# Performance work log

Hardware: AMD Instinct MI355X
Metric: run time of the kernel (lower is better)

The kernel has to match this reference:

```python
import jax, jax.numpy as jnp
import numpy as np

D_MODEL = 1024
TDS = 64
B, S = 8, 2048
DIN = D_MODEL + TDS   # 1088
DH = D_MODEL // 2     # 512


def setup_inputs() -> dict:
    key = jax.random.key(0)
    ks = jax.random.split(key, 6)
    sc = 1.0 / np.sqrt(DIN)
    return {
        "time_features": jax.random.normal(ks[0], (B, S, D_MODEL), jnp.float32),
        "env_info": jax.random.normal(ks[1], (B, TDS), jnp.float32),
        "Wq": jax.random.normal(ks[2], (DIN, DH), jnp.float32) * sc,
        "bq": jnp.zeros((DH,), jnp.float32),
        "Wk": jax.random.normal(ks[3], (DIN, DH), jnp.float32) * sc,
        "bk": jnp.zeros((DH,), jnp.float32),
        "Wv": jax.random.normal(ks[4], (DIN, DH), jnp.float32) * sc,
        "bv": jnp.zeros((DH,), jnp.float32),
        "Wg": jax.random.normal(ks[5], (DIN, 1), jnp.float32) * sc,
        "bg": jnp.zeros((1,), jnp.float32),
    }


def reference(time_features, env_info, Wq, bq, Wk, bk, Wv, bv, Wg, bg):
    b, s, _ = time_features.shape
    env = jnp.broadcast_to(env_info[:, None, :], (b, s, env_info.shape[-1]))
    x = jnp.concatenate([time_features, env], axis=2)  # [B,S,DIN]
    q = x @ Wq + bq                                    # [B,S,DH]
    k = x @ Wk + bk
    v = x @ Wv + bv
    gate = jax.nn.sigmoid(x @ Wg + bg)                 # [B,S,1]
    scores = jnp.einsum('bqd,bkd->bqk', q, k) / jnp.sqrt(jnp.float32(D_MODEL))
    gated = scores * gate                              # gate broadcasts over key dim
    attn = jax.nn.softmax(gated, axis=-1)
    return jnp.einsum('bqk,bkd->bqd', attn, v)         # [B,S,DH]
```

## Files before the change

kernel.cpp:

```cpp
#include <hip/hip_runtime.h>
#include <stdint.h>

typedef __attribute__((ext_vector_type(8))) __bf16 bf16x8;
typedef __attribute__((ext_vector_type(4))) __bf16 bf16x4;
typedef __attribute__((ext_vector_type(4))) float  f32x4;

#define DEV __device__ __forceinline__

DEV void gload16(const void* g, void* l) {
  __builtin_amdgcn_global_load_lds((const __attribute__((address_space(1))) uint32_t*)g,
                                   (__attribute__((address_space(3))) uint32_t*)l,
                                   16, 0, 0);
}

DEV f32x4 mfma16(bf16x8 a, bf16x8 b, f32x4 c) {
  return __builtin_amdgcn_mfma_f32_16x16x32_bf16(a, b, c, 0, 0, 0);
}

#define XB_OFF   0UL
#define S_OFF    0UL
#define Q_OFF    35651584UL
#define K_OFF    52428800UL
#define V_OFF    69206016UL
#define VT_OFF   85983232UL
#define WT_OFF   102760448UL
#define BIAS_OFF 106102784UL
#define GATE_OFF 106108928UL
#define S8_OFF   106174464UL

__global__ __launch_bounds__(256) void k_xbgate(
    const float* __restrict__ tf, const float* __restrict__ env,
    const float* __restrict__ Wg, const float* __restrict__ bg,
    __bf16* __restrict__ xb, float* __restrict__ gate) {
  const int row = blockIdx.x;
  const int t   = threadIdx.x;
  const int b   = row >> 11;
  const float4 v  = ((const float4*)(tf + (size_t)row * 1024))[t];
  const float4 wv = ((const float4*)Wg)[t];
  float dot = v.x * wv.x + v.y * wv.y + v.z * wv.z + v.w * wv.w;
  bf16x4 o; o.x = (__bf16)v.x; o.y = (__bf16)v.y; o.z = (__bf16)v.z; o.w = (__bf16)v.w;
  *(bf16x4*)(xb + (size_t)row * 1088 + t * 4) = o;
  if (t < 16) {
    const float4 e  = ((const float4*)(env + b * 64))[t];
    const float4 we = ((const float4*)Wg)[256 + t];
    dot += e.x * we.x + e.y * we.y + e.z * we.z + e.w * we.w;
    bf16x4 oe; oe.x = (__bf16)e.x; oe.y = (__bf16)e.y; oe.z = (__bf16)e.z; oe.w = (__bf16)e.w;
    *(bf16x4*)(xb + (size_t)row * 1088 + 1024 + t * 4) = oe;
  }
  #pragma unroll
  for (int m = 1; m < 64; m <<= 1) dot += __shfl_xor(dot, m, 64);
  __shared__ float red[4];
  if ((t & 63) == 0) red[t >> 6] = dot;
  __syncthreads();
  if (t == 0) {
    const float d = red[0] + red[1] + red[2] + red[3] + bg[0];
    gate[row] = 0.03125f / (1.0f + __expf(-d));
  }
}

__global__ __launch_bounds__(256) void k_wt(
    const float* __restrict__ Wq, const float* __restrict__ Wk, const float* __restrict__ Wv,
    const float* __restrict__ bq, const float* __restrict__ bk, const float* __restrict__ bv,
    __bf16* __restrict__ Wt, float* __restrict__ biasc) {
  __shared__ float tile[64][65];
  const int kt = blockIdx.x;
  const int ct = blockIdx.y;
  const int which = blockIdx.z;
  const float* W    = (which == 0) ? Wq : (which == 1) ? Wk : Wv;
  const float* bias = (which == 0) ? bq : (which == 1) ? bk : bv;
  const int t = threadIdx.x;
  const int k0 = kt * 64, c0 = ct * 64;
  #pragma unroll
  for (int j = 0; j < 4; ++j) {
    const int rr = (t >> 4) + j * 16;
    const float4 v4 = *(const float4*)(W + (size_t)(k0 + rr) * 512 + c0 + (t & 15) * 4);
    tile[rr][(t & 15) * 4 + 0] = v4.x;
    tile[rr][(t & 15) * 4 + 1] = v4.y;
    tile[rr][(t & 15) * 4 + 2] = v4.z;
    tile[rr][(t & 15) * 4 + 3] = v4.w;
  }
  if (kt == 0 && t < 64) biasc[which * 512 + c0 + t] = bias[c0 + t];
  __syncthreads();
  #pragma unroll
  for (int j = 0; j < 4; ++j) {
    const int nl = (t >> 4) + j * 16;
    const int kl = (t & 15) * 4;
    bf16x4 o;
    o.x = (__bf16)tile[kl + 0][nl];
    o.y = (__bf16)tile[kl + 1][nl];
    o.z = (__bf16)tile[kl + 2][nl];
    o.w = (__bf16)tile[kl + 3][nl];
    *(bf16x4*)(Wt + (size_t)(which * 512 + c0 + nl) * 1088 + k0 + kl) = o;
  }
}

__global__ __launch_bounds__(256, 3) void k_gemm(
    const __bf16* __restrict__ xb, const __bf16* __restrict__ Wt,
    const float* __restrict__ biasc, const float* __restrict__ gate,
    __bf16* __restrict__ q, __bf16* __restrict__ k, __bf16* __restrict__ v) {
  __shared__ alignas(16) __bf16 As[8192];
  __shared__ alignas(16) __bf16 Bs[8192];
  const int id = blockIdx.x;
  const int xcd = id & 7, local = id >> 3;
  const int bm = xcd * 16 + (local & 15);
  const int bn = local >> 4;
  const int tid = threadIdx.x, w = tid >> 6, lane = tid & 63;
  const int g = lane >> 4, l15 = lane & 15;
  const int wm = w >> 1, wn = w & 1;
  f32x4 acc[4][4] = {};
  const char* Ab = (const char*)(xb + (size_t)bm * 128 * 1088);
  const char* Bb = (const char*)(Wt + (size_t)bn * 128 * 1088);

  for (int kt = 0; kt < 17; ++kt) {
    const int k0b = kt * 128;
    #pragma unroll
    for (int i = 0; i < 4; ++i) {
      const int L = i * 4096 + w * 1024 + lane * 16;
      const int row = L >> 7;
      const int ch = (L >> 4) & 7;
      const int sch = ch ^ (row & 7);
      gload16(Ab + (size_t)row * 2176 + k0b + sch * 16, (char*)As + L);
      gload16(Bb + (size_t)row * 2176 + k0b + sch * 16, (char*)Bs + L);
    }
    __syncthreads();
    #pragma unroll
    for (int kk = 0; kk < 2; ++kk) {
      bf16x8 aF[4], bF[4];
      #pragma unroll
      for (int i = 0; i < 4; ++i) {
        const int rowa = wm * 64 + i * 16 + l15;
        const int cha = (kk * 4 + g) ^ (rowa & 7);
        aF[i] = *(const bf16x8*)((const char*)As + rowa * 128 + cha * 16);
        const int rowb = wn * 64 + i * 16 + l15;
        const int chb = (kk * 4 + g) ^ (rowb & 7);
        bF[i] = *(const bf16x8*)((const char*)Bs + rowb * 128 + chb * 16);
      }
      #pragma unroll
      for (int i = 0; i < 4; ++i)
        #pragma unroll
        for (int j = 0; j < 4; ++j)
          acc[i][j] = mfma16(aF[i], bF[j], acc[i][j]);
    }
    __syncthreads();
  }

  const int which = bn >> 2;
  __bf16* outp = (which == 0) ? q : (which == 1) ? k : v;
  const int ncolbase = bn * 128 + wn * 64 - which * 512;
  #pragma unroll
  for (int i = 0; i < 4; ++i) {
    #pragma unroll
    for (int r = 0; r < 4; ++r) {
      const int mrow = bm * 128 + wm * 64 + i * 16 + g * 4 + r;
      const float gt = (which == 0) ? gate[mrow] : 1.0f;
      #pragma unroll
      for (int j = 0; j < 4; ++j) {
        const int ncol = ncolbase + j * 16 + l15;
        float val = acc[i][j][r] + biasc[which * 512 + ncol];
        if (which == 0) val *= gt;
        outp[(size_t)mrow * 512 + ncol] = (__bf16)val;
      }
    }
  }
}

__global__ __launch_bounds__(256) void k_vtr(const __bf16* __restrict__ v,
                                             __bf16* __restrict__ vT) {
  __shared__ __bf16 tile[64][72];
  const int st = blockIdx.x, dt = blockIdx.y, b = blockIdx.z;
  const int t = threadIdx.x;
  {
    const int sl = t >> 2, dl = (t & 3) * 16;
    const __bf16* src = v + ((size_t)(b * 2048 + st * 64 + sl)) * 512 + dt * 64 + dl;
    *(bf16x8*)&tile[sl][dl]     = *(const bf16x8*)src;
    *(bf16x8*)&tile[sl][dl + 8] = *(const bf16x8*)(src + 8);
  }
  __syncthreads();
  {
    const int dl = t >> 2, sl = (t & 3) * 16;
    bf16x8 w0, w1;
    #pragma unroll
    for (int j = 0; j < 8; ++j) { w0[j] = tile[sl + j][dl]; w1[j] = tile[sl + 8 + j][dl]; }
    __bf16* dst = vT + ((size_t)(b * 512 + dt * 64 + dl)) * 2048 + st * 64 + sl;
    *(bf16x8*)dst = w0;
    *(bf16x8*)(dst + 8) = w1;
  }
}

template<int NB>
__global__ __launch_bounds__(256, 3) void k_sexp(
    const __bf16* __restrict__ q, const __bf16* __restrict__ kg,
    __bf16* __restrict__ S) {
  __shared__ alignas(16) __bf16 As[8192];
  __shared__ alignas(16) __bf16 Bs[8192];
  const int id = blockIdx.x;
  int batch, t;
  if (NB == 8) { batch = id & 7;        t = id >> 3; }
  else         { batch = (id & 7) >> 1; t = ((id >> 3) << 1) | (id & 1); }
  const int mt = t & 15, nt = t >> 4;
  const int tid = threadIdx.x, w = tid >> 6, lane = tid & 63;
  const int g = lane >> 4, l15 = lane & 15;
  const int wm = w >> 1, wn = w & 1;
  f32x4 acc[4][4] = {};
  const char* Ab = (const char*)(q  + ((size_t)batch * 2048 + mt * 128) * 512);
  const char* Bb = (const char*)(kg + ((size_t)batch * 2048 + nt * 128) * 512);

  for (int kt = 0; kt < 8; ++kt) {
    const int k0b = kt * 128;
    #pragma unroll
    for (int i = 0; i < 4; ++i) {
      const int L = i * 4096 + w * 1024 + lane * 16;
      const int row = L >> 7;
      const int ch = (L >> 4) & 7;
      const int sch = ch ^ (row & 7);
      gload16(Ab + (size_t)row * 1024 + k0b + sch * 16, (char*)As + L);
      gload16(Bb + (size_t)row * 1024 + k0b + sch * 16, (char*)Bs + L);
    }
    __syncthreads();
    #pragma unroll
    for (int kk = 0; kk < 2; ++kk) {
      bf16x8 aF[4], bF[4];
      #pragma unroll
      for (int i = 0; i < 4; ++i) {
        const int rowa = wm * 64 + i * 16 + l15;
        const int cha = (kk * 4 + g) ^ (rowa & 7);
        aF[i] = *(const bf16x8*)((const char*)As + rowa * 128 + cha * 16);
        const int rowb = wn * 64 + i * 16 + l15;
        const int chb = (kk * 4 + g) ^ (rowb & 7);
        bF[i] = *(const bf16x8*)((const char*)Bs + rowb * 128 + chb * 16);
      }
      #pragma unroll
      for (int i = 0; i < 4; ++i)
        #pragma unroll
        for (int j = 0; j < 4; ++j)
          acc[i][j] = mfma16(aF[i], bF[j], acc[i][j]);
    }
    __syncthreads();
  }

  __bf16* Srow = S + (size_t)batch * 2048 * 2048;
  #pragma unroll
  for (int i = 0; i < 4; ++i) {
    #pragma unroll
    for (int r = 0; r < 4; ++r) {
      const int mrow = mt * 128 + wm * 64 + i * 16 + g * 4 + r;
      #pragma unroll
      for (int j = 0; j < 4; ++j) {
        const int ncol = nt * 128 + wn * 64 + j * 16 + l15;
        Srow[(size_t)mrow * 2048 + ncol] = (__bf16)__expf(acc[i][j][r]);
      }
    }
  }
}

template<int NB>
__global__ __launch_bounds__(256, 2) void k_pv(
    const __bf16* __restrict__ S, const __bf16* __restrict__ vT,
    float* __restrict__ out) {
  __shared__ alignas(16) __bf16 As[4096];
  __shared__ alignas(16) __bf16 Bs[8192];
  const int id = blockIdx.x;
  int p, nt;
  if (NB == 8) { const int h = id >> 3; nt = h >> 5; p = (h & 31) * 8 + (id & 7); }
  else         { const int h = id >> 3; nt = h >> 4; p = (h & 15) * 8 + (id & 7); }
  const int batch = p >> 5, mt = p & 31;
  const int tid = threadIdx.x, w = tid >> 6, lane = tid & 63;
  const int g = lane >> 4, l15 = lane & 15;
  const int wm = w >> 1, wn = w & 1;
  f32x4 acc[2][4] = {};
  f32x4 l_acc[2] = {};
  bf16x8 ones;
  #pragma unroll
  for (int j = 0; j < 8; ++j) ones[j] = (__bf16)1.0f;

  const char* Ab = (const char*)(S  + ((size_t)batch * 2048 + mt * 64) * 2048);
  const char* Bb = (const char*)(vT + ((size_t)batch * 512 + nt * 128) * 2048);

  for (int kt = 0; kt < 32; ++kt) {
    const int k0b = kt * 128;
    #pragma unroll
    for (int i = 0; i < 2; ++i) {
      const int L = i * 4096 + tid * 16;
      const int row = L >> 7, ch = (L >> 4) & 7, sch = ch ^ (row & 7);
      gload16(Ab + (size_t)row * 4096 + k0b + sch * 16, (char*)As + L);
    }
    #pragma unroll
    for (int i = 0; i < 4; ++i) {
      const int L = i * 4096 + tid * 16;
      const int row = L >> 7, ch = (L >> 4) & 7, sch = ch ^ (row & 7);
      gload16(Bb + (size_t)row * 4096 + k0b + sch * 16, (char*)Bs + L);
    }
    __syncthreads();
    #pragma unroll
    for (int kk = 0; kk < 2; ++kk) {
      bf16x8 aF[2], bF[4];
      #pragma unroll
      for (int i = 0; i < 2; ++i) {
        const int rowa = wm * 32 + i * 16 + l15;
        const int cha = (kk * 4 + g) ^ (rowa & 7);
        aF[i] = *(const bf16x8*)((const char*)As + rowa * 128 + cha * 16);
      }
      #pragma unroll
      for (int j = 0; j < 4; ++j) {
        const int rowb = wn * 64 + j * 16 + l15;
        const int chb = (kk * 4 + g) ^ (rowb & 7);
        bF[j] = *(const bf16x8*)((const char*)Bs + rowb * 128 + chb * 16);
      }
      #pragma unroll
      for (int i = 0; i < 2; ++i) {
        #pragma unroll
        for (int j = 0; j < 4; ++j)
          acc[i][j] = mfma16(aF[i], bF[j], acc[i][j]);
        l_acc[i] = mfma16(aF[i], ones, l_acc[i]);
      }
    }
    __syncthreads();
  }

  #pragma unroll
  for (int i = 0; i < 2; ++i) {
    #pragma unroll
    for (int r = 0; r < 4; ++r) {
      const size_t mrow = (size_t)batch * 2048 + mt * 64 + wm * 32 + i * 16 + g * 4 + r;
      const float inv = 1.0f / l_acc[i][r];
      #pragma unroll
      for (int j = 0; j < 4; ++j) {
        const int ncol = nt * 128 + wn * 64 + j * 16 + l15;
        out[mrow * 512 + ncol] = acc[i][j][r] * inv;
      }
    }
  }
}

extern "C" void kernel_launch(void* const* d_in, const int* in_sizes, int n_in,
                              void* d_out, int out_size, void* d_ws, size_t ws_size,
                              hipStream_t stream) {
  const float* tf  = (const float*)d_in[0];
  const float* env = (const float*)d_in[1];
  const float* Wq  = (const float*)d_in[2];
  const float* bq  = (const float*)d_in[3];
  const float* Wk  = (const float*)d_in[4];
  const float* bk  = (const float*)d_in[5];
  const float* Wv  = (const float*)d_in[6];
  const float* bv  = (const float*)d_in[7];
  const float* Wg  = (const float*)d_in[8];
  const float* bg  = (const float*)d_in[9];
  float* out = (float*)d_out;
  char* ws = (char*)d_ws;

  __bf16* xb   = (__bf16*)(ws + XB_OFF);
  __bf16* Sbuf = (__bf16*)(ws + S_OFF);
  __bf16* qb   = (__bf16*)(ws + Q_OFF);
  __bf16* kb   = (__bf16*)(ws + K_OFF);
  __bf16* vb   = (__bf16*)(ws + V_OFF);
  __bf16* vT   = (__bf16*)(ws + VT_OFF);
  __bf16* Wt   = (__bf16*)(ws + WT_OFF);
  float* biasc = (float*)(ws + BIAS_OFF);
  float* gate  = (float*)(ws + GATE_OFF);

  k_xbgate<<<dim3(16384), dim3(256), 0, stream>>>(tf, env, Wg, bg, xb, gate);
  k_wt<<<dim3(17, 8, 3), dim3(256), 0, stream>>>(Wq, Wk, Wv, bq, bk, bv, Wt, biasc);
  k_gemm<<<dim3(1536), dim3(256), 0, stream>>>(xb, Wt, biasc, gate, qb, kb, vb);
  k_vtr<<<dim3(32, 8, 8), dim3(256), 0, stream>>>(vb, vT);

  if (ws_size >= S8_OFF + 67108864UL) {
    __bf16* S8 = (__bf16*)(ws + S8_OFF);
    k_sexp<8><<<dim3(2048), dim3(256), 0, stream>>>(qb, kb, S8);
    k_pv<8>  <<<dim3(1024), dim3(256), 0, stream>>>(S8, vT, out);
  } else {
    const size_t hb = 4UL * 2048 * 512;
    const size_t hv = 4UL * 512 * 2048;
    const size_t ho = 4UL * 2048 * 512;
    k_sexp<4><<<dim3(1024), dim3(256), 0, stream>>>(qb, kb, Sbuf);
    k_pv<4>  <<<dim3(512),  dim3(256), 0, stream>>>(Sbuf, vT, out);
    k_sexp<4><<<dim3(1024), dim3(256), 0, stream>>>(qb + hb, kb + hb, Sbuf);
    k_pv<4>  <<<dim3(512),  dim3(256), 0, stream>>>(Sbuf, vT + hv, out + ho);
  }
}
```

Baseline: 179.5 us.

## Fold env projection into per-batch bias, fuse V transpose into GEMM, enlarge PV tiles

The env features are constant per batch, so their contribution to Q/K/V (plus the biases) is now computed once per batch by a small kernel and added in the GEMM epilogue. This shrinks the projection GEMM's K dimension from 1088 to 1024 and stops writing env columns into the bf16 activation buffer. The V output is transposed through shared memory inside the GEMM epilogue and written straight to vT, which removes the separate transpose kernel and the round trip through an intermediate V buffer. The PV kernel now uses 128x128 tiles instead of 64x128 and launches half as many blocks, giving more reuse per block at the cost of more registers per thread and fewer blocks in flight.

```diff
diff --git a/kernel.cpp b/kernel.cpp
--- a/kernel.cpp
+++ b/kernel.cpp
@@ -19,19 +19,18 @@
 
 #define XB_OFF   0UL
 #define S_OFF    0UL
-#define Q_OFF    35651584UL
-#define K_OFF    52428800UL
-#define V_OFF    69206016UL
-#define VT_OFF   85983232UL
-#define WT_OFF   102760448UL
-#define BIAS_OFF 106102784UL
-#define GATE_OFF 106108928UL
-#define S8_OFF   106174464UL
+#define Q_OFF    33554432UL
+#define K_OFF    50331648UL
+#define VT_OFF   67108864UL
+#define WT_OFF   83886080UL
+#define ENVQ_OFF 87031808UL
+#define GATE_OFF 87080960UL
+#define S8_OFF   87146496UL
 
 __global__ __launch_bounds__(256) void k_xbgate(
     const float* __restrict__ tf, const float* __restrict__ env,
     const float* __restrict__ Wg, const float* __restrict__ bg,
-    __bf16* __restrict__ xb, float* __restrict__ gate) {
+    __bf16* __restrict__ xbb, float* __restrict__ gate) {
   const int row = blockIdx.x;
   const int t   = threadIdx.x;
   const int b   = row >> 11;
@@ -39,13 +38,11 @@
   const float4 wv = ((const float4*)Wg)[t];
   float dot = v.x * wv.x + v.y * wv.y + v.z * wv.z + v.w * wv.w;
   bf16x4 o; o.x = (__bf16)v.x; o.y = (__bf16)v.y; o.z = (__bf16)v.z; o.w = (__bf16)v.w;
-  *(bf16x4*)(xb + (size_t)row * 1088 + t * 4) = o;
+  *(bf16x4*)(xbb + (size_t)row * 1024 + t * 4) = o;
   if (t < 16) {
     const float4 e  = ((const float4*)(env + b * 64))[t];
     const float4 we = ((const float4*)Wg)[256 + t];
     dot += e.x * we.x + e.y * we.y + e.z * we.z + e.w * we.w;
-    bf16x4 oe; oe.x = (__bf16)e.x; oe.y = (__bf16)e.y; oe.z = (__bf16)e.z; oe.w = (__bf16)e.w;
-    *(bf16x4*)(xb + (size_t)row * 1088 + 1024 + t * 4) = oe;
   }
   #pragma unroll
   for (int m = 1; m < 64; m <<= 1) dot += __shfl_xor(dot, m, 64);
@@ -60,14 +57,12 @@
 
 __global__ __launch_bounds__(256) void k_wt(
     const float* __restrict__ Wq, const float* __restrict__ Wk, const float* __restrict__ Wv,
-    const float* __restrict__ bq, const float* __restrict__ bk, const float* __restrict__ bv,
-    __bf16* __restrict__ Wt, float* __restrict__ biasc) {
+    __bf16* __restrict__ Wt) {
   __shared__ float tile[64][65];
   const int kt = blockIdx.x;
   const int ct = blockIdx.y;
   const int which = blockIdx.z;
-  const float* W    = (which == 0) ? Wq : (which == 1) ? Wk : Wv;
-  const float* bias = (which == 0) ? bq : (which == 1) ? bk : bv;
+  const float* W = (which == 0) ? Wq : (which == 1) ? Wk : Wv;
   const int t = threadIdx.x;
   const int k0 = kt * 64, c0 = ct * 64;
   #pragma unroll
@@ -79,7 +74,6 @@
     tile[rr][(t & 15) * 4 + 2] = v4.z;
     tile[rr][(t & 15) * 4 + 3] = v4.w;
   }
-  if (kt == 0 && t < 64) biasc[which * 512 + c0 + t] = bias[c0 + t];
   __syncthreads();
   #pragma unroll
   for (int j = 0; j < 4; ++j) {
@@ -90,16 +84,34 @@
     o.y = (__bf16)tile[kl + 1][nl];
     o.z = (__bf16)tile[kl + 2][nl];
     o.w = (__bf16)tile[kl + 3][nl];
-    *(bf16x4*)(Wt + (size_t)(which * 512 + c0 + nl) * 1088 + k0 + kl) = o;
-  }
+    *(bf16x4*)(Wt + (size_t)(which * 512 + c0 + nl) * 1024 + k0 + kl) = o;
+  }
+}
+
+__global__ __launch_bounds__(256) void k_envq(
+    const float* __restrict__ env,
+    const float* __restrict__ Wq, const float* __restrict__ Wk, const float* __restrict__ Wv,
+    const float* __restrict__ bq, const float* __restrict__ bk, const float* __restrict__ bv,
+    float* __restrict__ envq) {
+  const int n = blockIdx.x * 256 + threadIdx.x;
+  const int b = blockIdx.y;
+  const int which = n >> 9, col = n & 511;
+  const float* W    = (which == 0) ? Wq : (which == 1) ? Wk : Wv;
+  const float* bias = (which == 0) ? bq : (which == 1) ? bk : bv;
+  float s = bias[col];
+  #pragma unroll 8
+  for (int kk = 0; kk < 64; ++kk)
+    s += env[b * 64 + kk] * W[(size_t)(1024 + kk) * 512 + col];
+  envq[b * 1536 + n] = s;
 }
 
 __global__ __launch_bounds__(256, 3) void k_gemm(
-    const __bf16* __restrict__ xb, const __bf16* __restrict__ Wt,
-    const float* __restrict__ biasc, const float* __restrict__ gate,
-    __bf16* __restrict__ q, __bf16* __restrict__ k, __bf16* __restrict__ v) {
-  __shared__ alignas(16) __bf16 As[8192];
-  __shared__ alignas(16) __bf16 Bs[8192];
+    const __bf16* __restrict__ xbb, const __bf16* __restrict__ Wt,
+    const float* __restrict__ envq, const float* __restrict__ gate,
+    __bf16* __restrict__ q, __bf16* __restrict__ k, __bf16* __restrict__ vT) {
+  __shared__ alignas(16) __bf16 SM[16384];
+  __bf16* As = SM;
+  __bf16* Bs = SM + 8192;
   const int id = blockIdx.x;
   const int xcd = id & 7, local = id >> 3;
   const int bm = xcd * 16 + (local & 15);
@@ -108,10 +120,10 @@
   const int g = lane >> 4, l15 = lane & 15;
   const int wm = w >> 1, wn = w & 1;
   f32x4 acc[4][4] = {};
-  const char* Ab = (const char*)(xb + (size_t)bm * 128 * 1088);
-  const char* Bb = (const char*)(Wt + (size_t)bn * 128 * 1088);
-
-  for (int kt = 0; kt < 17; ++kt) {
+  const char* Ab = (const char*)(xbb + (size_t)bm * 128 * 1024);
+  const char* Bb = (const char*)(Wt + (size_t)bn * 128 * 1024);
+
+  for (int kt = 0; kt < 16; ++kt) {
     const int k0b = kt * 128;
     #pragma unroll
     for (int i = 0; i < 4; ++i) {
@@ -119,8 +131,8 @@
       const int row = L >> 7;
       const int ch = (L >> 4) & 7;
       const int sch = ch ^ (row & 7);
-      gload16(Ab + (size_t)row * 2176 + k0b + sch * 16, (char*)As + L);
-      gload16(Bb + (size_t)row * 2176 + k0b + sch * 16, (char*)Bs + L);
+      gload16(Ab + (size_t)row * 2048 + k0b + sch * 16, (char*)As + L);
+      gload16(Bb + (size_t)row * 2048 + k0b + sch * 16, (char*)Bs + L);
     }
     __syncthreads();
     #pragma unroll
@@ -145,45 +157,53 @@
   }
 
   const int which = bn >> 2;
-  __bf16* outp = (which == 0) ? q : (which == 1) ? k : v;
-  const int ncolbase = bn * 128 + wn * 64 - which * 512;
-  #pragma unroll
-  for (int i = 0; i < 4; ++i) {
-    #pragma unroll
-    for (int r = 0; r < 4; ++r) {
-      const int mrow = bm * 128 + wm * 64 + i * 16 + g * 4 + r;
-      const float gt = (which == 0) ? gate[mrow] : 1.0f;
-      #pragma unroll
-      for (int j = 0; j < 4; ++j) {
-        const int ncol = ncolbase + j * 16 + l15;
-        float val = acc[i][j][r] + biasc[which * 512 + ncol];
-        if (which == 0) val *= gt;
-        outp[(size_t)mrow * 512 + ncol] = (__bf16)val;
-      }
-    }
-  }
-}
-
-__global__ __launch_bounds__(256) void k_vtr(const __bf16* __restrict__ v,
-                                             __bf16* __restrict__ vT) {
-  __shared__ __bf16 tile[64][72];
-  const int st = blockIdx.x, dt = blockIdx.y, b = blockIdx.z;
-  const int t = threadIdx.x;
-  {
-    const int sl = t >> 2, dl = (t & 3) * 16;
-    const __bf16* src = v + ((size_t)(b * 2048 + st * 64 + sl)) * 512 + dt * 64 + dl;
-    *(bf16x8*)&tile[sl][dl]     = *(const bf16x8*)src;
-    *(bf16x8*)&tile[sl][dl + 8] = *(const bf16x8*)(src + 8);
-  }
-  __syncthreads();
-  {
-    const int dl = t >> 2, sl = (t & 3) * 16;
-    bf16x8 w0, w1;
-    #pragma unroll
-    for (int j = 0; j < 8; ++j) { w0[j] = tile[sl + j][dl]; w1[j] = tile[sl + 8 + j][dl]; }
-    __bf16* dst = vT + ((size_t)(b * 512 + dt * 64 + dl)) * 2048 + st * 64 + sl;
-    *(bf16x8*)dst = w0;
-    *(bf16x8*)(dst + 8) = w1;
+  const int batch = bm >> 4;
+  if (which < 2) {
+    __bf16* outp = (which == 0) ? q : k;
+    const int ncolbase = bn * 128 + wn * 64 - which * 512;
+    #pragma unroll
+    for (int i = 0; i < 4; ++i) {
+      #pragma unroll
+      for (int r = 0; r < 4; ++r) {
+        const int mrow = bm * 128 + wm * 64 + i * 16 + g * 4 + r;
+        const float gt = (which == 0) ? gate[mrow] : 1.0f;
+        #pragma unroll
+        for (int j = 0; j < 4; ++j) {
+          const int ncol = ncolbase + j * 16 + l15;
+          float val = acc[i][j][r] + envq[batch * 1536 + bn * 128 + wn * 64 + j * 16 + l15];
+          if (which == 0) val *= gt;
+          outp[(size_t)mrow * 512 + ncol] = (__bf16)val;
+        }
+      }
+    }
+  } else {
+    #pragma unroll
+    for (int j = 0; j < 4; ++j) {
+      const int ncol = wn * 64 + j * 16 + l15;
+      const float bv = envq[batch * 1536 + bn * 128 + ncol];
+      const int sw = (ncol & 7) << 3;
+      #pragma unroll
+      for (int i = 0; i < 4; ++i) {
+        const int mbase = wm * 64 + i * 16 + g * 4;
+        bf16x4 pk;
+        pk.x = (__bf16)(acc[i][j][0] + bv);
+        pk.y = (__bf16)(acc[i][j][1] + bv);
+        pk.z = (__bf16)(acc[i][j][2] + bv);
+        pk.w = (__bf16)(acc[i][j][3] + bv);
+        *(bf16x4*)(SM + ncol * 128 + (mbase ^ sw)) = pk;
+      }
+    }
+    __syncthreads();
+    const int colL = tid & 127, h = tid >> 7;
+    const __bf16* src = SM + colL * 128;
+    const int sw = (colL & 7) << 3;
+    __bf16* dst = vT + ((size_t)batch * 512 + (bn - 8) * 128 + colL) * 2048
+                     + (bm & 15) * 128 + h * 64;
+    #pragma unroll
+    for (int c = 0; c < 8; ++c) {
+      const int m0 = h * 64 + c * 8;
+      *(bf16x8*)(dst + c * 8) = *(const bf16x8*)(src + (m0 ^ sw));
+    }
   }
 }
 
@@ -254,60 +274,51 @@
 }
 
 template<int NB>
-__global__ __launch_bounds__(256, 2) void k_pv(
+__global__ __launch_bounds__(256, 3) void k_pv(
     const __bf16* __restrict__ S, const __bf16* __restrict__ vT,
     float* __restrict__ out) {
-  __shared__ alignas(16) __bf16 As[4096];
+  __shared__ alignas(16) __bf16 As[8192];
   __shared__ alignas(16) __bf16 Bs[8192];
   const int id = blockIdx.x;
-  int p, nt;
-  if (NB == 8) { const int h = id >> 3; nt = h >> 5; p = (h & 31) * 8 + (id & 7); }
-  else         { const int h = id >> 3; nt = h >> 4; p = (h & 15) * 8 + (id & 7); }
-  const int batch = p >> 5, mt = p & 31;
+  int batch, mt, nt;
+  if (NB == 8) { batch = id & 7; const int h = id >> 3; mt = h & 15; nt = h >> 4; }
+  else { batch = (id & 7) >> 1; const int h = ((id >> 3) << 1) | (id & 1); mt = h & 15; nt = h >> 4; }
   const int tid = threadIdx.x, w = tid >> 6, lane = tid & 63;
   const int g = lane >> 4, l15 = lane & 15;
   const int wm = w >> 1, wn = w & 1;
-  f32x4 acc[2][4] = {};
-  f32x4 l_acc[2] = {};
+  f32x4 acc[4][4] = {};
+  f32x4 l_acc[4] = {};
   bf16x8 ones;
   #pragma unroll
   for (int j = 0; j < 8; ++j) ones[j] = (__bf16)1.0f;
 
-  const char* Ab = (const char*)(S  + ((size_t)batch * 2048 + mt * 64) * 2048);
+  const char* Ab = (const char*)(S  + ((size_t)batch * 2048 + mt * 128) * 2048);
   const char* Bb = (const char*)(vT + ((size_t)batch * 512 + nt * 128) * 2048);
 
   for (int kt = 0; kt < 32; ++kt) {
     const int k0b = kt * 128;
     #pragma unroll
-    for (int i = 0; i < 2; ++i) {
-      const int L = i * 4096 + tid * 16;
+    for (int i = 0; i < 4; ++i) {
+      const int L = i * 4096 + w * 1024 + lane * 16;
       const int row = L >> 7, ch = (L >> 4) & 7, sch = ch ^ (row & 7);
       gload16(Ab + (size_t)row * 4096 + k0b + sch * 16, (char*)As + L);
-    }
-    #pragma unroll
-    for (int i = 0; i < 4; ++i) {
-      const int L = i * 4096 + tid * 16;
-      const int row = L >> 7, ch = (L >> 4) & 7, sch = ch ^ (row & 7);
       gload16(Bb + (size_t)row * 4096 + k0b + sch * 16, (char*)Bs + L);
     }
     __syncthreads();
     #pragma unroll
     for (int kk = 0; kk < 2; ++kk) {
-      bf16x8 aF[2], bF[4];
-      #pragma unroll
-      for (int i = 0; i < 2; ++i) {
-        const int rowa = wm * 32 + i * 16 + l15;
+      bf16x8 aF[4], bF[4];
+      #pragma unroll
+      for (int i = 0; i < 4; ++i) {
+        const int rowa = wm * 64 + i * 16 + l15;
         const int cha = (kk * 4 + g) ^ (rowa & 7);
         aF[i] = *(const bf16x8*)((const char*)As + rowa * 128 + cha * 16);
-      }
-      #pragma unroll
-      for (int j = 0; j < 4; ++j) {
-        const int rowb = wn * 64 + j * 16 + l15;
+        const int rowb = wn * 64 + i * 16 + l15;
         const int chb = (kk * 4 + g) ^ (rowb & 7);
-        bF[j] = *(const bf16x8*)((const char*)Bs + rowb * 128 + chb * 16);
-      }
-      #pragma unroll
-      for (int i = 0; i < 2; ++i) {
+        bF[i] = *(const bf16x8*)((const char*)Bs + rowb * 128 + chb * 16);
+      }
+      #pragma unroll
+      for (int i = 0; i < 4; ++i) {
         #pragma unroll
         for (int j = 0; j < 4; ++j)
           acc[i][j] = mfma16(aF[i], bF[j], acc[i][j]);
@@ -318,10 +329,10 @@
   }
 
   #pragma unroll
-  for (int i = 0; i < 2; ++i) {
+  for (int i = 0; i < 4; ++i) {
     #pragma unroll
     for (int r = 0; r < 4; ++r) {
-      const size_t mrow = (size_t)batch * 2048 + mt * 64 + wm * 32 + i * 16 + g * 4 + r;
+      const size_t mrow = (size_t)batch * 2048 + mt * 128 + wm * 64 + i * 16 + g * 4 + r;
       const float inv = 1.0f / l_acc[i][r];
       #pragma unroll
       for (int j = 0; j < 4; ++j) {
@@ -348,32 +359,31 @@
   float* out = (float*)d_out;
   char* ws = (char*)d_ws;
 
-  __bf16* xb   = (__bf16*)(ws + XB_OFF);
+  __bf16* xbb  = (__bf16*)(ws + XB_OFF);
   __bf16* Sbuf = (__bf16*)(ws + S_OFF);
   __bf16* qb   = (__bf16*)(ws + Q_OFF);
   __bf16* kb   = (__bf16*)(ws + K_OFF);
-  __bf16* vb   = (__bf16*)(ws + V_OFF);
   __bf16* vT   = (__bf16*)(ws + VT_OFF);
   __bf16* Wt   = (__bf16*)(ws + WT_OFF);
-  float* biasc = (float*)(ws + BIAS_OFF);
+  float* envq  = (float*)(ws + ENVQ_OFF);
   float* gate  = (float*)(ws + GATE_OFF);
 
-  k_xbgate<<<dim3(16384), dim3(256), 0, stream>>>(tf, env, Wg, bg, xb, gate);
-  k_wt<<<dim3(17, 8, 3), dim3(256), 0, stream>>>(Wq, Wk, Wv, bq, bk, bv, Wt, biasc);
-  k_gemm<<<dim3(1536), dim3(256), 0, stream>>>(xb, Wt, biasc, gate, qb, kb, vb);
-  k_vtr<<<dim3(32, 8, 8), dim3(256), 0, stream>>>(vb, vT);
+  k_xbgate<<<dim3(16384), dim3(256), 0, stream>>>(tf, env, Wg, bg, xbb, gate);
+  k_wt<<<dim3(16, 8, 3), dim3(256), 0, stream>>>(Wq, Wk, Wv, Wt);
+  k_envq<<<dim3(6, 8), dim3(256), 0, stream>>>(env, Wq, Wk, Wv, bq, bk, bv, envq);
+  k_gemm<<<dim3(1536), dim3(256), 0, stream>>>(xbb, Wt, envq, gate, qb, kb, vT);
 
   if (ws_size >= S8_OFF + 67108864UL) {
     __bf16* S8 = (__bf16*)(ws + S8_OFF);
     k_sexp<8><<<dim3(2048), dim3(256), 0, stream>>>(qb, kb, S8);
-    k_pv<8>  <<<dim3(1024), dim3(256), 0, stream>>>(S8, vT, out);
+    k_pv<8>  <<<dim3(512),  dim3(256), 0, stream>>>(S8, vT, out);
   } else {
     const size_t hb = 4UL * 2048 * 512;
     const size_t hv = 4UL * 512 * 2048;
     const size_t ho = 4UL * 2048 * 512;
     k_sexp<4><<<dim3(1024), dim3(256), 0, stream>>>(qb, kb, Sbuf);
-    k_pv<4>  <<<dim3(512),  dim3(256), 0, stream>>>(Sbuf, vT, out);
+    k_pv<4>  <<<dim3(256),  dim3(256), 0, stream>>>(Sbuf, vT, out);
     k_sexp<4><<<dim3(1024), dim3(256), 0, stream>>>(qb + hb, kb + hb, Sbuf);
-    k_pv<4>  <<<dim3(512),  dim3(256), 0, stream>>>(Sbuf, vT + hv, out + ho);
-  }
-}
+    k_pv<4>  <<<dim3(256),  dim3(256), 0, stream>>>(Sbuf, vT + hv, out + ho);
+  }
+}
```

Result: faster. 162.9 us (-9.2%).
